# Kernel tuning notes

Measured on AMD Instinct MI355X. Metric: run time of the kernel, lower is better.

## Reference

```python
import jax, jax.numpy as jnp
import numpy as np

B, H, W = 2, 32, 128
HW = H * W
N, C = 4096, 64
KQ, KN = 32, 16          # nsample_q, nsample
DIST = 10.0              # neighbor distance threshold
NEG = -1e10


def _knn(q, p, k):
    # q: (B,M,3), p: (B,N,3) -> idx (B,M,k), sqdist (B,M,k)
    sqd = jnp.sum((q[:, :, None, :] - p[:, None, :, :]) ** 2, axis=-1)
    neg, idx = jax.lax.top_k(-sqd, k)
    return idx, -neg


def _gather(p, idx):
    # p: (B,N,C), idx: (B,M,K) -> (B,M,K,C)
    return jax.vmap(lambda a, i: a[i])(p, idx)


def _norm_feat(x):
    # per-point channel normalization, torch.std default is unbiased (ddof=1)
    m = jnp.mean(x, axis=-1, keepdims=True)
    s = jnp.clip(jnp.std(x, axis=-1, keepdims=True, ddof=1), 1e-12)
    return (x - m) / s


def _conv(x, w, b, g, e):
    # 1x1 conv + BatchNorm (track_running_stats=False -> batch stats) + LeakyReLU(0.1)
    y = jnp.einsum('bnkc,cd->bnkd', x, w) + b
    mu = y.mean(axis=(0, 1, 2), keepdims=True)
    var = y.var(axis=(0, 1, 2), keepdims=True)
    y = (y - mu) * jax.lax.rsqrt(var + 1e-5) * g + e
    return jnp.where(y > 0, y, 0.1 * y)


def setup_inputs() -> dict:
    key = jax.random.key(0)
    ks = jax.random.split(key, 20)
    inp = {
        'xyz_proj_raw': jax.random.normal(ks[0], (B, H, W, 3), jnp.float32),
        'warped_xyz': jax.random.normal(ks[1], (B, HW, 3), jnp.float32),
        'warped_points': jax.random.normal(ks[2], (B, HW, C), jnp.float32),
        'idx_n2': jax.random.randint(ks[3], (B, HW, 2), 0, W),
        'f2_xyz': jax.random.normal(ks[4], (B, N, 3), jnp.float32),
        'f2_points': jax.random.normal(ks[5], (B, N, C), jnp.float32),
        'lidar_z': jax.random.uniform(ks[6], (B, HW, 1), jnp.float32),
    }
    shapes = {
        'm1w0': (70, 128), 'm1w1': (128, 64), 'piw': (6, 64),
        'm2w0': (128, 64), 'm2w1': (64, 64), 'pcw': (10, 64),
        'm3w0': (192, 64), 'm3w1': (64, 64),
    }
    i = 7
    for name, shp in shapes.items():
        inp[name] = jax.random.normal(ks[i], shp, jnp.float32) * 0.05
        i += 1
        pre = name[:-2] if name[-2] == 'w' else name[:-1]
        suf = name[-1] if name[-2] == 'w' else ''
        cout = shp[1]
        inp[pre + 'b' + suf] = jnp.zeros((cout,), jnp.float32)
        inp[pre + 'g' + suf] = jnp.ones((cout,), jnp.float32)
        inp[pre + 'e' + suf] = jnp.zeros((cout,), jnp.float32)
    return inp


def reference(xyz_proj_raw, warped_xyz, warped_points, idx_n2, f2_xyz, f2_points, lidar_z,
              m1w0, m1b0, m1g0, m1e0, m1w1, m1b1, m1g1, m1e1,
              piw, pib, pig, pie,
              m2w0, m2b0, m2g0, m2e0, m2w1, m2b1, m2g1, m2e1,
              pcw, pcb, pcg, pce,
              m3w0, m3b0, m3g0, m3e0, m3w1, m3b1, m3g1, m3e1):
    # ---- stage 1: cross kNN grouping into image features ----
    idx_q, _ = _knn(warped_xyz, f2_xyz, KQ)
    qi_xyz = _gather(f2_xyz, idx_q)          # (B,HW,KQ,3)
    qi_pts = _gather(f2_points, idx_q)       # (B,HW,KQ,C)

    wxyz = warped_xyz * lidar_z              # (B,HW,3)
    pi_xyz_exp = jnp.broadcast_to(wxyz[:, :, None, :], (B, HW, KQ, 3))
    pi_pts_exp = jnp.broadcast_to(warped_points[:, :, None, :], (B, HW, KQ, C))
    pi_xyz_diff_concat = jnp.concatenate([pi_xyz_exp, qi_xyz], axis=3)  # (B,HW,KQ,6)

    pi_feat_diff = _norm_feat(pi_pts_exp) * _norm_feat(qi_pts)          # correlation
    feat = jnp.concatenate([pi_xyz_diff_concat, pi_feat_diff], axis=3)  # (B,HW,KQ,70)

    feat = _conv(feat, m1w0, m1b0, m1g0, m1e0)
    feat = _conv(feat, m1w1, m1b1, m1g1, m1e1)                          # (B,HW,KQ,64)
    pi_enc = _conv(pi_xyz_diff_concat, piw, pib, pig, pie)              # (B,HW,KQ,64)

    pi_cat = jnp.concatenate([pi_enc, feat], axis=3)
    pi_cat = _conv(pi_cat, m2w0, m2b0, m2g0, m2e0)
    pi_cat = _conv(pi_cat, m2w1, m2b1, m2g1, m2e1)
    WQ = jax.nn.softmax(pi_cat, axis=2)
    pi_feat1 = jnp.sum(WQ * feat, axis=2)                               # (B,HW,64)

    # ---- stage 2: self kNN (use_trans=False -> raw projected xyz), thresholded validity ----
    xyz_pr = xyz_proj_raw.reshape(B, HW, 3)
    idx2, sqd2 = _knn(xyz_pr, xyz_pr, KN)
    valid = (sqd2 < DIST * DIST).astype(pi_feat1.dtype)[..., None]      # (B,HW,KN,1)

    pc_xyz_g = _gather(wxyz, idx2)                                      # (B,HW,KN,3)
    pc_pts_g = _gather(pi_feat1, idx2)                                  # (B,HW,KN,64)
    pc_xyz_new = jnp.broadcast_to(wxyz[:, :, None, :], (B, HW, KN, 3))
    pc_pts_new = jnp.broadcast_to(warped_points[:, :, None, :], (B, HW, KN, C))

    pc_diff = pc_xyz_g - pc_xyz_new
    pc_euc = jnp.sqrt(jnp.sum(pc_diff * pc_diff, axis=3, keepdims=True) + 1e-20)
    pc_xyz_cat = jnp.concatenate([pc_xyz_new, pc_xyz_g, pc_diff, pc_euc], axis=3)  # 10ch

    pc_enc = _conv(pc_xyz_cat, pcw, pcb, pcg, pce)
    pc_cat = jnp.concatenate([pc_enc, pc_pts_new, pc_pts_g], axis=-1)   # (B,HW,KN,192)
    pc_cat = _conv(pc_cat, m3w0, m3b0, m3g0, m3e0)
    pc_cat = _conv(pc_cat, m3w1, m3b1, m3g1, m3e1)

    pc_cat = pc_cat * valid + NEG * (1.0 - valid)
    WP = jax.nn.softmax(pc_cat, axis=2)
    out = jnp.sum(WP * pc_pts_g, axis=2)                                # (B,HW,64)
    return out.reshape(B, H, W, -1)
```

## Files before the change

kernel.cpp:

```cpp
#include <hip/hip_runtime.h>
#include <math.h>

constexpr int Bn  = 2;
constexpr int HWn = 4096;
constexpr int Nn  = 4096;
constexpr int KQn = 32;
constexpr int KNn = 16;
constexpr float INV_R1 = 1.0f/262144.0f;
constexpr float INV_R2 = 1.0f/131072.0f;

typedef _Float16 f16x8 __attribute__((ext_vector_type(8)));
typedef _Float16 f16x2 __attribute__((ext_vector_type(2)));
typedef float    f32x4 __attribute__((ext_vector_type(4)));

__device__ __forceinline__ float wred64(float v){
  #pragma unroll
  for (int m = 32; m > 0; m >>= 1) v += __shfl_xor(v, m, 64);
  return v;
}
__device__ __forceinline__ float leakyf(float v){ return v > 0.f ? v : 0.1f*v; }

__device__ __forceinline__ void bn_param(const float* st, int c, float inv_n,
                                         const float* g, const float* e,
                                         float& sc, float& sh){
  float mu  = st[c]*inv_n;
  float var = st[128+c]*inv_n - mu*mu;
  float s   = g[c]*rsqrtf(var + 1e-5f);
  sc = s; sh = e[c] - mu*s;
}

__device__ __forceinline__ void build_x70(int row,
    const float* __restrict__ wxyz, const float* __restrict__ f2_xyz,
    const float* __restrict__ normW, const float* __restrict__ normF2,
    const int* __restrict__ idxq, float* x){
  int p = row >> 5;
  int b = p >> 12;
  int idx = idxq[row];
  const float* wx = wxyz + (size_t)p*3;
  const float* fx = f2_xyz + ((size_t)b*Nn + idx)*3;
  x[0]=wx[0]; x[1]=wx[1]; x[2]=wx[2];
  x[3]=fx[0]; x[4]=fx[1]; x[5]=fx[2];
  const float4* nw = (const float4*)(normW  + (size_t)p*64);
  const float4* nf = (const float4*)(normF2 + ((size_t)b*Nn + idx)*64);
  #pragma unroll
  for (int c=0;c<16;c++){
    float4 a = nw[c], q = nf[c];
    x[6+4*c+0]=a.x*q.x; x[6+4*c+1]=a.y*q.y; x[6+4*c+2]=a.z*q.z; x[6+4*c+3]=a.w*q.w;
  }
}

__device__ __forceinline__ void build_x10(int row,
    const float* __restrict__ wxyz, const int* __restrict__ idx2, float* x){
  int p = row >> 4, b = p >> 12;
  int idx = idx2[row];
  const float* nw = wxyz + (size_t)p*3;
  const float* gw = wxyz + ((size_t)b*HWn + idx)*3;
  float n0=nw[0],n1=nw[1],n2=nw[2];
  float g0=gw[0],g1=gw[1],g2=gw[2];
  float d0=g0-n0, d1=g1-n1, d2=g2-n2;
  x[0]=n0;x[1]=n1;x[2]=n2; x[3]=g0;x[4]=g1;x[5]=g2;
  x[6]=d0;x[7]=d1;x[8]=d2; x[9]=sqrtf(d0*d0+d1*d1+d2*d2+1e-20f);
}

__global__ __launch_bounds__(256) void k_knn_prep(
    const float* __restrict__ qA, const float* __restrict__ pA, int* __restrict__ oA,
    const float* __restrict__ qB, const float* __restrict__ pB, int* __restrict__ oB,
    float* __restrict__ ovalid,
    const float* __restrict__ lidar_z,
    const float* __restrict__ warped_points, const float* __restrict__ f2_points,
    const float* __restrict__ m1w0, const float* __restrict__ m1w1,
    const float* __restrict__ piw, const float* __restrict__ pcw,
    const float* __restrict__ m2w0, const float* __restrict__ m2w1,
    const float* __restrict__ m3w0, const float* __restrict__ m3w1,
    float* __restrict__ wxyz, float* __restrict__ normW, float* __restrict__ normF2,
    float* __restrict__ piwT, float* __restrict__ pcwT,
    _Float16* __restrict__ w1h, _Float16* __restrict__ w2h,
    _Float16* __restrict__ w3h, _Float16* __restrict__ w4h,
    _Float16* __restrict__ w5h, _Float16* __restrict__ w6h)
{
  int bid = blockIdx.x;
  int tid = threadIdx.x;
  if (bid >= 16384){
    int blk = bid - 16384;
    if (blk < 4096){
      int lane = tid & 63;
      int p = blk*4 + (tid >> 6);
      const float* src; float* dst;
      if (p < Bn*HWn){ src = warped_points + (size_t)p*64; dst = normW + (size_t)p*64; }
      else { int q = p - Bn*HWn; src = f2_points + (size_t)q*64; dst = normF2 + (size_t)q*64; }
      float x = src[lane];
      float m = wred64(x) * (1.f/64.f);
      float d = x - m;
      float ss = wred64(d*d);
      float s = fmaxf(sqrtf(ss*(1.f/63.f)), 1e-12f);
      dst[lane] = d / s;
    } else if (blk < 4192){
      int e = (blk-4096)*256 + tid;
      wxyz[e] = qA[e] * lidar_z[e/3];
    } else if (blk < 4196){
      int e = (blk-4192)*256 + tid;
      if (e < 384){ piwT[(e & 63)*6  + (e >> 6)] = piw[e]; }
      else if (e < 1024){ int f = e-384; pcwT[(f & 63)*10 + (f >> 6)] = pcw[f]; }
    } else {
      int e = (blk-4196)*256 + tid;
      if (e < 12288){
        int j = e/96, k = e - j*96;
        w1h[e] = (k < 70) ? (_Float16)m1w0[k*128 + j] : (_Float16)0.f;
      } else if (e < 20480){
        int f = e - 12288; int d = f >> 7, c = f & 127;
        w2h[f] = (_Float16)m1w1[c*64 + d];
      } else if (e < 28672){
        int f = e - 20480; int d = f >> 7, c = f & 127;
        w3h[f] = (_Float16)m2w0[c*64 + d];
      } else if (e < 32768){
        int f = e - 28672; int d = f >> 6, c = f & 63;
        w4h[f] = (_Float16)m2w1[c*64 + d];
      } else if (e < 45056){
        int f = e - 32768; int d = f/192, c = f - 192*d;
        w5h[f] = (_Float16)m3w0[c*64 + d];
      } else {
        int f = e - 45056; int d = f >> 6, c = f & 63;
        w6h[f] = (_Float16)m3w1[c*64 + d];
      }
    }
    return;
  }
  __shared__ int hist[4096];
  __shared__ int wsum[4];
  __shared__ unsigned int redm[4], redM[4];
  __shared__ int sh_sel, sh_rem, sh_cls, cnt_lt, cnt_eq;
  bool second = bid >= 8192;
  int blk = second ? (bid - 8192) : bid;
  int K = second ? KNn : KQn;
  const float* qpts = second ? qB : qA;
  const float* pts  = second ? pB : pA;
  int* oidx = second ? oB : oA;
  int b = blk >> 12;
  int qi = blk & 4095;
  int lane = tid & 63, wv = tid >> 6;
  const float* qp = qpts + ((size_t)(b*HWn+qi))*3;
  float qx=qp[0], qy=qp[1], qz=qp[2];
  const float* pb = pts + (size_t)b*Nn*3;
  unsigned int key[16];
  {
    const float4* pb4 = (const float4*)(pb + (size_t)tid*48);
    float4 v[12];
    #pragma unroll
    for (int i=0;i<12;i++) v[i] = pb4[i];
    const float* f = (const float*)v;
    #pragma unroll
    for (int i=0;i<16;i++){
      float dx = __fsub_rn(qx, f[i*3+0]);
      float dy = __fsub_rn(qy, f[i*3+1]);
      float dz = __fsub_rn(qz, f[i*3+2]);
      float d2 = __fadd_rn(__fadd_rn(__fmul_rn(dx,dx), __fmul_rn(dy,dy)), __fmul_rn(dz,dz));
      key[i] = __float_as_uint(d2);
    }
  }
  {
    int4 z = {0,0,0,0};
    #pragma unroll
    for (int j=0;j<4;j++) ((int4*)hist)[tid + j*256] = z;
  }
  unsigned int mn = key[0], mx = key[0];
  #pragma unroll
  for (int i=1;i<16;i++){ mn = min(mn, key[i]); mx = max(mx, key[i]); }
  #pragma unroll
  for (int m=32;m>0;m>>=1){
    mn = min(mn, (unsigned int)__shfl_xor((int)mn, m, 64));
    mx = max(mx, (unsigned int)__shfl_xor((int)mx, m, 64));
  }
  if (lane == 0){ redm[wv] = mn; redM[wv] = mx; }
  if (tid == 0){ cnt_lt = 0; cnt_eq = 0; }
  __syncthreads();
  mn = min(min(redm[0],redm[1]), min(redm[2],redm[3]));
  mx = max(max(redM[0],redM[1]), max(redM[2],redM[3]));
  unsigned int R = mx - mn;
  int L = (R == 0u) ? 0 : (31 - __clz(R));
  int shift = (L > 11) ? (L - 11) : 0;
  #pragma unroll
  for (int i=0;i<16;i++){
    unsigned int d = ((key[i]-mn) >> shift) & 4095u;
    int slot = (int)(((d & 15u) << 8) | (d >> 4));
    atomicAdd(&hist[slot], 1);
  }
  __syncthreads();
  {
    int hv[16]; int tot = 0;
    #pragma unroll
    for (int i=0;i<16;i++){ hv[i] = hist[tid + i*256]; tot += hv[i]; }
    int pref = tot;
    #pragma unroll
    for (int m=1;m<64;m<<=1){ int t = __shfl_up(pref, m, 64); if (lane >= m) pref += t; }
    if (lane == 63) wsum[wv] = pref;
    __syncthreads();
    int off = 0;
    #pragma unroll
    for (int i=0;i<3;i++) if (i < wv) off += wsum[i];
    pref += off;
    if (pref >= K && (pref - tot) < K){
      int running = pref - tot;
      bool done = false;
      #pragma unroll
      for (int i=0;i<16;i++){
        if (!done && running + hv[i] >= K){
          sh_sel = tid*16 + i;
          sh_rem = K - running;
          sh_cls = hv[i];
          done = true;
        }
        if (!done) running += hv[i];
      }
    }
  }
  __syncthreads();
  unsigned int sel = (unsigned int)sh_sel;
  int rem = sh_rem, cls = sh_cls;
  int nless = K - rem;
  size_t obase = ((size_t)(b*HWn+qi))*K;
  const unsigned int U100 = __float_as_uint(100.0f);
  #pragma unroll
  for (int i=0;i<16;i++){
    unsigned int d = ((key[i]-mn) >> shift) & 4095u;
    if (d < sel){
      int s = atomicAdd(&cnt_lt, 1);
      oidx[obase+s] = tid*16 + i;
      if (second) ovalid[obase+s] = (key[i] < U100) ? 1.f : 0.f;
    } else if (d == sel){
      int s = atomicAdd(&cnt_eq, 1);
      if (s < 2048){ hist[s] = (int)key[i]; hist[2048+s] = tid*16 + i; }
    }
  }
  __syncthreads();
  if (wv == 0){
    int cc = cls < 2048 ? cls : 2048;
    for (int c = lane; c < cc; c += 64){
      unsigned int kc = (unsigned int)hist[c];
      int ic = hist[2048+c];
      int rank = 0;
      for (int j = 0; j < cc; j++){
        unsigned int kj = (unsigned int)hist[j];
        if (kj < kc || (kj == kc && hist[2048+j] < ic)) rank++;
      }
      if (rank < rem){
        oidx[obase + nless + rank] = ic;
        if (second) ovalid[obase + nless + rank] = (kc < U100) ? 1.f : 0.f;
      }
    }
  }
}

__global__ __launch_bounds__(256) void k_build_stats(
    const float* __restrict__ wxyz, const float* __restrict__ f2_xyz,
    const float* __restrict__ normW, const float* __restrict__ normF2,
    const int* __restrict__ idxq, const int* __restrict__ idx2,
    const _Float16* __restrict__ w1h,
    _Float16* __restrict__ X1, float* stats, float* __restrict__ gram)
{
  __shared__ float ssum[128], sssq[128];
  __shared__ float sacc[66];
  int blk = blockIdx.x, tid = threadIdx.x, lane = tid & 63;
  if (blk < 1024){
    int row = blk*256 + tid;
    {
      float x[70];
      build_x70(row, wxyz, f2_xyz, normW, normF2, idxq, x);
      unsigned int* d32 = (unsigned int*)(X1 + (size_t)row*96);
      union { unsigned int u; _Float16 h[2]; } pk;
      #pragma unroll
      for (int c=0;c<35;c++){
        pk.h[0] = (_Float16)x[2*c]; pk.h[1] = (_Float16)x[2*c+1];
        d32[c] = pk.u;
      }
      #pragma unroll
      for (int c=35;c<48;c++) d32[c] = 0u;
    }
    if (tid < 128){ ssum[tid]=0.f; sssq[tid]=0.f; }
    __syncthreads();
    int wave = tid >> 6;
    int quad = lane >> 4, n16 = lane & 15;
    float r1[8], r2[8];
    #pragma unroll
    for (int i=0;i<8;i++){ r1[i]=0.f; r2[i]=0.f; }
    for (int t=0;t<4;t++){
      int m0 = blk*256 + t*64 + wave*16;
      const _Float16* xr = X1 + (size_t)(m0 + n16)*96 + quad*8;
      f16x8 a0 = *(const f16x8*)(xr);
      f16x8 a1 = *(const f16x8*)(xr + 32);
      f16x8 a2 = *(const f16x8*)(xr + 64);
      #pragma unroll
      for (int nt = 0; nt < 8; nt++){
        const _Float16* wr = w1h + (size_t)(nt*16 + n16)*96 + quad*8;
        f16x8 b0 = *(const f16x8*)(wr);
        f16x8 b1 = *(const f16x8*)(wr + 32);
        f16x8 b2 = *(const f16x8*)(wr + 64);
        f32x4 acc = {0.f,0.f,0.f,0.f};
        acc = __builtin_amdgcn_mfma_f32_16x16x32_f16(a0, b0, acc, 0,0,0);
        acc = __builtin_amdgcn_mfma_f32_16x16x32_f16(a1, b1, acc, 0,0,0);
        acc = __builtin_amdgcn_mfma_f32_16x16x32_f16(a2, b2, acc, 0,0,0);
        float s1 = acc[0]+acc[1]+acc[2]+acc[3];
        float s2 = acc[0]*acc[0]+acc[1]*acc[1]+acc[2]*acc[2]+acc[3]*acc[3];
        s1 += __shfl_xor(s1, 16, 64); s1 += __shfl_xor(s1, 32, 64);
        s2 += __shfl_xor(s2, 16, 64); s2 += __shfl_xor(s2, 32, 64);
        r1[nt] += s1; r2[nt] += s2;
      }
    }
    if (quad == 0){
      #pragma unroll
      for (int nt=0;nt<8;nt++){
        atomicAdd(&ssum[nt*16+n16], r1[nt]); atomicAdd(&sssq[nt*16+n16], r2[nt]);
      }
    }
    __syncthreads();
    if (tid < 128){ atomicAdd(&stats[tid], ssum[tid]); atomicAdd(&stats[128+tid], sssq[tid]); }
  } else if (blk < 1088){
    float a[28];
    #pragma unroll
    for (int q=0;q<28;q++) a[q]=0.f;
    int g = (blk-1024)*256 + tid;
    for (int s=0;s<16;s++){
      int row = g + s*16384;
      int p = row >> 5, b = p >> 12;
      int idx = idxq[row];
      const float* wx = wxyz + (size_t)p*3;
      const float* fx = f2_xyz + ((size_t)b*Nn + idx)*3;
      float xt[7] = {wx[0],wx[1],wx[2],fx[0],fx[1],fx[2],1.f};
      int q=0;
      #pragma unroll
      for (int i=0;i<7;i++)
        #pragma unroll
        for (int j=i;j<7;j++) a[q++] += xt[i]*xt[j];
    }
    if (tid < 28) sacc[tid]=0.f;
    __syncthreads();
    #pragma unroll
    for (int q=0;q<28;q++){
      float v = wred64(a[q]);
      if (lane==0) atomicAdd(&sacc[q], v);
    }
    __syncthreads();
    if (tid < 28) atomicAdd(&gram[tid], sacc[tid]);
  } else {
    float a[66];
    #pragma unroll
    for (int q=0;q<66;q++) a[q]=0.f;
    int g = (blk-1088)*256 + tid;
    for (int s=0;s<16;s++){
      int row = g + s*8192;
      float x[10];
      build_x10(row, wxyz, idx2, x);
      float xt[11] = {x[0],x[1],x[2],x[3],x[4],x[5],x[6],x[7],x[8],x[9],1.f};
      int q=0;
      #pragma unroll
      for (int i=0;i<11;i++)
        #pragma unroll
        for (int j=i;j<11;j++) a[q++] += xt[i]*xt[j];
    }
    if (tid < 66) sacc[tid]=0.f;
    __syncthreads();
    #pragma unroll
    for (int q=0;q<66;q++){
      float v = wred64(a[q]);
      if (lane==0) atomicAdd(&sacc[q], v);
    }
    __syncthreads();
    if (tid < 66) atomicAdd(&gram[32+tid], sacc[tid]);
  }
}

__global__ __launch_bounds__(256) void k_mfma_m1(
    const _Float16* __restrict__ X1, const _Float16* __restrict__ w1h,
    const _Float16* __restrict__ w2h,
    const float* __restrict__ m1g0, const float* __restrict__ m1e0,
    float* stats, _Float16* __restrict__ y2h,
    const float* __restrict__ gram,
    const float* __restrict__ piw, const float* __restrict__ pib,
    const float* __restrict__ pcw, const float* __restrict__ pcb)
{
  if (blockIdx.x >= 1024){
    int tid = threadIdx.x;
    if (tid < 64){
      int c = tid;
      float wt[7];
      #pragma unroll
      for (int i=0;i<6;i++) wt[i] = piw[i*64+c];
      wt[6] = pib[c];
      const float* G = gram;
      float sum=0.f, ssq=0.f;
      #pragma unroll
      for (int i=0;i<7;i++){
        int offi = i*7 - (i*(i-1))/2;
        sum += wt[i]*G[offi + (6-i)];
        #pragma unroll
        for (int j=0;j<7;j++){
          int ii = i<j? i : j, jj = i<j? j : i;
          int o = ii*7 - (ii*(ii-1))/2 + (jj-ii);
          ssq += wt[i]*wt[j]*G[o];
        }
      }
      stats[2*256+c] = sum; stats[2*256+128+c] = ssq;
    } else if (tid < 128){
      int c = tid-64;
      float wt[11];
      #pragma unroll
      for (int i=0;i<10;i++) wt[i] = pcw[i*64+c];
      wt[10] = pcb[c];
      const float* G = gram + 32;
      float sum=0.f, ssq=0.f;
      #pragma unroll
      for (int i=0;i<11;i++){
        int offi = i*11 - (i*(i-1))/2;
        sum += wt[i]*G[offi + (10-i)];
        #pragma unroll
        for (int j=0;j<11;j++){
          int ii = i<j? i : j, jj = i<j? j : i;
          int o = ii*11 - (ii*(ii-1))/2 + (jj-ii);
          ssq += wt[i]*wt[j]*G[o];
        }
      }
      stats[5*256+c] = sum; stats[5*256+128+c] = ssq;
    }
    return;
  }
  __shared__ _Float16 st[64*136];
  __shared__ float sc1[128], sh1[128], ssum[64], sssq[64];
  int tid = threadIdx.x;
  if (tid < 128){
    float s,h; bn_param(stats, tid, INV_R1, m1g0, m1e0, s, h);
    sc1[tid]=s; sh1[tid]=h;
  }
  if (tid < 64){ ssum[tid]=0.f; sssq[tid]=0.f; }
  __syncthreads();
  int wave = tid >> 6, lane = tid & 63;
  int quad = lane >> 4, n16 = lane & 15;
  float r1[4], r2[4];
  #pragma unroll
  for (int i=0;i<4;i++){ r1[i]=0.f; r2[i]=0.f; }
  for (int t=0;t<4;t++){
    int m0 = blockIdx.x*256 + t*64 + wave*16;
    const _Float16* xr = X1 + (size_t)(m0 + n16)*96 + quad*8;
    f16x8 a0 = *(const f16x8*)(xr);
    f16x8 a1 = *(const f16x8*)(xr + 32);
    f16x8 a2 = *(const f16x8*)(xr + 64);
    #pragma unroll
    for (int nt = 0; nt < 8; nt++){
      const _Float16* wr = w1h + (size_t)(nt*16 + n16)*96 + quad*8;
      f16x8 b0 = *(const f16x8*)(wr);
      f16x8 b1 = *(const f16x8*)(wr + 32);
      f16x8 b2 = *(const f16x8*)(wr + 64);
      f32x4 acc = {0.f,0.f,0.f,0.f};
      acc = __builtin_amdgcn_mfma_f32_16x16x32_f16(a0, b0, acc, 0,0,0);
      acc = __builtin_amdgcn_mfma_f32_16x16x32_f16(a1, b1, acc, 0,0,0);
      acc = __builtin_amdgcn_mfma_f32_16x16x32_f16(a2, b2, acc, 0,0,0);
      int ch = nt*16 + n16;
      float sc = sc1[ch], sh = sh1[ch];
      #pragma unroll
      for (int r=0;r<4;r++){
        float v = leakyf(acc[r]*sc + sh);
        st[(size_t)(wave*16 + quad*4 + r)*136 + ch] = (_Float16)v;
      }
    }
    __syncthreads();
    const _Float16* tr = st + (size_t)(wave*16 + n16)*136 + quad*8;
    f16x8 t0 = *(const f16x8*)(tr);
    f16x8 t1 = *(const f16x8*)(tr + 32);
    f16x8 t2 = *(const f16x8*)(tr + 64);
    f16x8 t3 = *(const f16x8*)(tr + 96);
    #pragma unroll
    for (int nt = 0; nt < 4; nt++){
      const _Float16* wr = w2h + (size_t)(nt*16 + n16)*128 + quad*8;
      f16x8 b0 = *(const f16x8*)(wr);
      f16x8 b1 = *(const f16x8*)(wr + 32);
      f16x8 b2 = *(const f16x8*)(wr + 64);
      f16x8 b3 = *(const f16x8*)(wr + 96);
      f32x4 acc = {0.f,0.f,0.f,0.f};
      acc = __builtin_amdgcn_mfma_f32_16x16x32_f16(t0, b0, acc, 0,0,0);
      acc = __builtin_amdgcn_mfma_f32_16x16x32_f16(t1, b1, acc, 0,0,0);
      acc = __builtin_amdgcn_mfma_f32_16x16x32_f16(t2, b2, acc, 0,0,0);
      acc = __builtin_amdgcn_mfma_f32_16x16x32_f16(t3, b3, acc, 0,0,0);
      int ch = nt*16 + n16;
      #pragma unroll
      for (int r=0;r<4;r++){
        int rowg = blockIdx.x*256 + t*64 + wave*16 + quad*4 + r;
        y2h[(size_t)rowg*64 + ch] = (_Float16)acc[r];
      }
      float s1 = acc[0]+acc[1]+acc[2]+acc[3];
      float s2 = acc[0]*acc[0]+acc[1]*acc[1]+acc[2]*acc[2]+acc[3]*acc[3];
      s1 += __shfl_xor(s1, 16, 64); s1 += __shfl_xor(s1, 32, 64);
      s2 += __shfl_xor(s2, 16, 64); s2 += __shfl_xor(s2, 32, 64);
      r1[nt] += s1; r2[nt] += s2;
    }
    __syncthreads();
  }
  if (quad == 0){
    #pragma unroll
    for (int nt=0;nt<4;nt++){
      atomicAdd(&ssum[nt*16+n16], r1[nt]); atomicAdd(&sssq[nt*16+n16], r2[nt]);
    }
  }
  __syncthreads();
  if (tid < 64){ atomicAdd(&stats[1*256+tid], ssum[tid]); atomicAdd(&stats[1*256+128+tid], sssq[tid]); }
}

__global__ __launch_bounds__(256) void k_mfma_m2a(
    const float* __restrict__ wxyz, const float* __restrict__ f2_xyz,
    const int* __restrict__ idxq,
    const float* __restrict__ piwT, const float* __restrict__ pib,
    const float* __restrict__ pig, const float* __restrict__ pie,
    const float* __restrict__ m1g1, const float* __restrict__ m1e1,
    const _Float16* __restrict__ y2h, const _Float16* __restrict__ w3h,
    float* stats, _Float16* __restrict__ y3h)
{
  __shared__ _Float16 su[64*136];
  __shared__ float spw[384];
  __shared__ float scp[64], shp[64], sc2[64], sh2[64], ssum[64], sssq[64];
  int tid = threadIdx.x;
  for (int d = tid; d < 384; d += 256) spw[d] = piwT[d];
  if (tid < 64){
    float s,h;
    bn_param(stats+2*256, tid, INV_R1, pig,  pie,  s, h); scp[tid]=s; shp[tid]=h;
    bn_param(stats+1*256, tid, INV_R1, m1g1, m1e1, s, h); sc2[tid]=s; sh2[tid]=h;
    ssum[tid]=0.f; sssq[tid]=0.f;
  }
  __syncthreads();
  int r = tid & 63, cg = tid >> 6;
  int wave = tid >> 6, lane = tid & 63, quad = lane >> 4, n16 = lane & 15;
  float r1[4], r2[4];
  #pragma unroll
  for (int i=0;i<4;i++){ r1[i]=0.f; r2[i]=0.f; }
  for (int t=0;t<4;t++){
    int rowg = blockIdx.x*256 + t*64 + r;
    {
      int p = rowg >> 5, b = p >> 12;
      int idx = idxq[rowg];
      const float* wx = wxyz + (size_t)p*3;
      const float* fx = f2_xyz + ((size_t)b*Nn + idx)*3;
      float x0=wx[0],x1=wx[1],x2=wx[2],x3=fx[0],x4=fx[1],x5=fx[2];
      #pragma unroll
      for (int jj=0;jj<16;jj++){
        int j = cg*16 + jj;
        const float* pw = spw + j*6;
        float e = pib[j] + x0*pw[0]+x1*pw[1]+x2*pw[2]+x3*pw[3]+x4*pw[4]+x5*pw[5];
        su[r*136 + j] = (_Float16)leakyf(e*scp[j] + shp[j]);
      }
      const f16x8* yr = (const f16x8*)(y2h + (size_t)rowg*64 + cg*16);
      f16x8 q0 = yr[0], q1 = yr[1];
      #pragma unroll
      for (int jj=0;jj<8;jj++){
        int c = cg*16 + jj;
        su[r*136 + 64 + c] = (_Float16)leakyf((float)q0[jj]*sc2[c] + sh2[c]);
      }
      #pragma unroll
      for (int jj=0;jj<8;jj++){
        int c = cg*16 + 8 + jj;
        su[r*136 + 64 + c] = (_Float16)leakyf((float)q1[jj]*sc2[c] + sh2[c]);
      }
    }
    __syncthreads();
    const _Float16* ur = su + (size_t)(wave*16 + n16)*136 + quad*8;
    f16x8 a0 = *(const f16x8*)(ur);
    f16x8 a1 = *(const f16x8*)(ur + 32);
    f16x8 a2 = *(const f16x8*)(ur + 64);
    f16x8 a3 = *(const f16x8*)(ur + 96);
    #pragma unroll
    for (int nt = 0; nt < 4; nt++){
      const _Float16* wr = w3h + (size_t)(nt*16 + n16)*128 + quad*8;
      f16x8 b0 = *(const f16x8*)(wr);
      f16x8 b1 = *(const f16x8*)(wr + 32);
      f16x8 b2 = *(const f16x8*)(wr + 64);
      f16x8 b3 = *(const f16x8*)(wr + 96);
      f32x4 acc = {0.f,0.f,0.f,0.f};
      acc = __builtin_amdgcn_mfma_f32_16x16x32_f16(a0, b0, acc, 0,0,0);
      acc = __builtin_amdgcn_mfma_f32_16x16x32_f16(a1, b1, acc, 0,0,0);
      acc = __builtin_amdgcn_mfma_f32_16x16x32_f16(a2, b2, acc, 0,0,0);
      acc = __builtin_amdgcn_mfma_f32_16x16x32_f16(a3, b3, acc, 0,0,0);
      int ch = nt*16 + n16;
      #pragma unroll
      for (int rr=0;rr<4;rr++){
        int rg = blockIdx.x*256 + t*64 + wave*16 + quad*4 + rr;
        y3h[(size_t)rg*64 + ch] = (_Float16)acc[rr];
      }
      float s1 = acc[0]+acc[1]+acc[2]+acc[3];
      float s2 = acc[0]*acc[0]+acc[1]*acc[1]+acc[2]*acc[2]+acc[3]*acc[3];
      s1 += __shfl_xor(s1, 16, 64); s1 += __shfl_xor(s1, 32, 64);
      s2 += __shfl_xor(s2, 16, 64); s2 += __shfl_xor(s2, 32, 64);
      r1[nt] += s1; r2[nt] += s2;
    }
    __syncthreads();
  }
  if (quad == 0){
    #pragma unroll
    for (int nt=0;nt<4;nt++){
      atomicAdd(&ssum[nt*16+n16], r1[nt]); atomicAdd(&sssq[nt*16+n16], r2[nt]);
    }
  }
  __syncthreads();
  if (tid < 64){ atomicAdd(&stats[3*256+tid], ssum[tid]); atomicAdd(&stats[3*256+128+tid], sssq[tid]); }
}

__global__ __launch_bounds__(256) void k_mfma_pw64(
    const _Float16* __restrict__ yin, const _Float16* __restrict__ wh,
    const float* __restrict__ g, const float* __restrict__ e,
    const float* statsIn, float* statsOut, float inv_n,
    _Float16* __restrict__ yout)
{
  __shared__ _Float16 stt[64*72];
  __shared__ float sc[64], sh[64], ssum[64], sssq[64];
  int tid = threadIdx.x;
  if (tid < 64){
    float s,h; bn_param(statsIn, tid, inv_n, g, e, s, h);
    sc[tid]=s; sh[tid]=h; ssum[tid]=0.f; sssq[tid]=0.f;
  }
  __syncthreads();
  int r = tid & 63, cg = tid >> 6;
  int wave = tid >> 6, lane = tid & 63, quad = lane >> 4, n16 = lane & 15;
  float r1[4], r2[4];
  #pragma unroll
  for (int i=0;i<4;i++){ r1[i]=0.f; r2[i]=0.f; }
  for (int t=0;t<4;t++){
    int rowg = blockIdx.x*256 + t*64 + r;
    const f16x8* yr = (const f16x8*)(yin + (size_t)rowg*64 + cg*16);
    f16x8 q0 = yr[0], q1 = yr[1];
    #pragma unroll
    for (int jj=0;jj<8;jj++){
      int c = cg*16 + jj;
      stt[r*72 + c] = (_Float16)leakyf((float)q0[jj]*sc[c] + sh[c]);
    }
    #pragma unroll
    for (int jj=0;jj<8;jj++){
      int c = cg*16 + 8 + jj;
      stt[r*72 + c] = (_Float16)leakyf((float)q1[jj]*sc[c] + sh[c]);
    }
    __syncthreads();
    const _Float16* tr = stt + (size_t)(wave*16 + n16)*72 + quad*8;
    f16x8 a0 = *(const f16x8*)(tr);
    f16x8 a1 = *(const f16x8*)(tr + 32);
    #pragma unroll
    for (int nt = 0; nt < 4; nt++){
      const _Float16* wr = wh + (size_t)(nt*16 + n16)*64 + quad*8;
      f16x8 b0 = *(const f16x8*)(wr);
      f16x8 b1 = *(const f16x8*)(wr + 32);
      f32x4 acc = {0.f,0.f,0.f,0.f};
      acc = __builtin_amdgcn_mfma_f32_16x16x32_f16(a0, b0, acc, 0,0,0);
      acc = __builtin_amdgcn_mfma_f32_16x16x32_f16(a1, b1, acc, 0,0,0);
      int ch = nt*16 + n16;
      #pragma unroll
      for (int rr=0;rr<4;rr++){
        int rg = blockIdx.x*256 + t*64 + wave*16 + quad*4 + rr;
        yout[(size_t)rg*64 + ch] = (_Float16)acc[rr];
      }
      float s1 = acc[0]+acc[1]+acc[2]+acc[3];
      float s2 = acc[0]*acc[0]+acc[1]*acc[1]+acc[2]*acc[2]+acc[3]*acc[3];
      s1 += __shfl_xor(s1, 16, 64); s1 += __shfl_xor(s1, 32, 64);
      s2 += __shfl_xor(s2, 16, 64); s2 += __shfl_xor(s2, 32, 64);
      r1[nt] += s1; r2[nt] += s2;
    }
    __syncthreads();
  }
  if (quad == 0){
    #pragma unroll
    for (int nt=0;nt<4;nt++){
      atomicAdd(&ssum[nt*16+n16], r1[nt]); atomicAdd(&sssq[nt*16+n16], r2[nt]);
    }
  }
  __syncthreads();
  if (tid < 64){ atomicAdd(&statsOut[tid], ssum[tid]); atomicAdd(&statsOut[128+tid], sssq[tid]); }
}

__global__ __launch_bounds__(256) void k_mfma_m3a(
    const float* __restrict__ wxyz, const float* __restrict__ warped_points,
    const _Float16* __restrict__ pif1h, const int* __restrict__ idx2,
    const float* __restrict__ pcwT, const float* __restrict__ pcb,
    const float* __restrict__ pcg, const float* __restrict__ pce,
    const _Float16* __restrict__ w5h,
    float* stats, _Float16* __restrict__ y5h)
{
  __shared__ _Float16 sv[64*200];
  __shared__ float spw[640];
  __shared__ float scp[64], shp[64], ssum[64], sssq[64];
  int tid = threadIdx.x;
  for (int d = tid; d < 640; d += 256) spw[d] = pcwT[d];
  if (tid < 64){
    float s,h; bn_param(stats+5*256, tid, INV_R2, pcg, pce, s, h);
    scp[tid]=s; shp[tid]=h; ssum[tid]=0.f; sssq[tid]=0.f;
  }
  __syncthreads();
  int r = tid & 63, cg = tid >> 6;
  int wave = tid >> 6, lane = tid & 63, quad = lane >> 4, n16 = lane & 15;
  float r1[4], r2[4];
  #pragma unroll
  for (int i=0;i<4;i++){ r1[i]=0.f; r2[i]=0.f; }
  for (int t=0;t<4;t++){
    int rowg = blockIdx.x*256 + t*64 + r;
    {
      int p = rowg >> 4, b = p >> 12;
      int idx = idx2[rowg];
      float x[10];
      build_x10(rowg, wxyz, idx2, x);
      #pragma unroll
      for (int jj=0;jj<16;jj++){
        int j = cg*16 + jj;
        const float* pw = spw + j*10;
        float e = pcb[j];
        #pragma unroll
        for (int i=0;i<10;i++) e += x[i]*pw[i];
        sv[r*200 + j] = (_Float16)leakyf(e*scp[j] + shp[j]);
      }
      const float4* wp = (const float4*)(warped_points + (size_t)p*64 + cg*16);
      #pragma unroll
      for (int v4=0; v4<4; v4++){
        float4 q = wp[v4];
        int c = 64 + cg*16 + v4*4;
        sv[r*200 + c + 0] = (_Float16)q.x;
        sv[r*200 + c + 1] = (_Float16)q.y;
        sv[r*200 + c + 2] = (_Float16)q.z;
        sv[r*200 + c + 3] = (_Float16)q.w;
      }
      const f16x8* pg = (const f16x8*)(pif1h + ((size_t)(b*HWn) + idx)*64 + cg*16);
      f16x8 g0 = pg[0], g1 = pg[1];
      #pragma unroll
      for (int jj=0;jj<8;jj++) sv[r*200 + 128 + cg*16 + jj] = g0[jj];
      #pragma unroll
      for (int jj=0;jj<8;jj++) sv[r*200 + 136 + cg*16 + jj] = g1[jj];
    }
    __syncthreads();
    const _Float16* vr = sv + (size_t)(wave*16 + n16)*200 + quad*8;
    f16x8 a0 = *(const f16x8*)(vr);
    f16x8 a1 = *(const f16x8*)(vr + 32);
    f16x8 a2 = *(const f16x8*)(vr + 64);
    f16x8 a3 = *(const f16x8*)(vr + 96);
    f16x8 a4 = *(const f16x8*)(vr + 128);
    f16x8 a5 = *(const f16x8*)(vr + 160);
    #pragma unroll
    for (int nt = 0; nt < 4; nt++){
      const _Float16* wr = w5h + (size_t)(nt*16 + n16)*192 + quad*8;
      f32x4 acc = {0.f,0.f,0.f,0.f};
      acc = __builtin_amdgcn_mfma_f32_16x16x32_f16(a0, *(const f16x8*)(wr),       acc, 0,0,0);
      acc = __builtin_amdgcn_mfma_f32_16x16x32_f16(a1, *(const f16x8*)(wr + 32),  acc, 0,0,0);
      acc = __builtin_amdgcn_mfma_f32_16x16x32_f16(a2, *(const f16x8*)(wr + 64),  acc, 0,0,0);
      acc = __builtin_amdgcn_mfma_f32_16x16x32_f16(a3, *(const f16x8*)(wr + 96),  acc, 0,0,0);
      acc = __builtin_amdgcn_mfma_f32_16x16x32_f16(a4, *(const f16x8*)(wr + 128), acc, 0,0,0);
      acc = __builtin_amdgcn_mfma_f32_16x16x32_f16(a5, *(const f16x8*)(wr + 160), acc, 0,0,0);
      int ch = nt*16 + n16;
      #pragma unroll
      for (int rr=0;rr<4;rr++){
        int rg = blockIdx.x*256 + t*64 + wave*16 + quad*4 + rr;
        y5h[(size_t)rg*64 + ch] = (_Float16)acc[rr];
      }
      float s1 = acc[0]+acc[1]+acc[2]+acc[3];
      float s2 = acc[0]*acc[0]+acc[1]*acc[1]+acc[2]*acc[2]+acc[3]*acc[3];
      s1 += __shfl_xor(s1, 16, 64); s1 += __shfl_xor(s1, 32, 64);
      s2 += __shfl_xor(s2, 16, 64); s2 += __shfl_xor(s2, 32, 64);
      r1[nt] += s1; r2[nt] += s2;
    }
    __syncthreads();
  }
  if (quad == 0){
    #pragma unroll
    for (int nt=0;nt<4;nt++){
      atomicAdd(&ssum[nt*16+n16], r1[nt]); atomicAdd(&sssq[nt*16+n16], r2[nt]);
    }
  }
  __syncthreads();
  if (tid < 64){ atomicAdd(&stats[6*256+tid], ssum[tid]); atomicAdd(&stats[6*256+128+tid], sssq[tid]); }
}

__global__ __launch_bounds__(256) void k_softmax1(
    const _Float16* __restrict__ y2h, const _Float16* __restrict__ y4h,
    const float* stats,
    const float* __restrict__ m1g1, const float* __restrict__ m1e1,
    const float* __restrict__ m2g1, const float* __restrict__ m2e1,
    _Float16* __restrict__ pif1h)
{
  int tid = threadIdx.x;
  int p  = blockIdx.x*8 + (tid >> 5);
  int dp = tid & 31;
  int d0 = 2*dp, d1 = 2*dp + 1;
  float sc2a,sh2a,sc4a,sh4a, sc2b,sh2b,sc4b,sh4b;
  bn_param(stats+1*256, d0, INV_R1, m1g1, m1e1, sc2a, sh2a);
  bn_param(stats+4*256, d0, INV_R1, m2g1, m2e1, sc4a, sh4a);
  bn_param(stats+1*256, d1, INV_R1, m1g1, m1e1, sc2b, sh2b);
  bn_param(stats+4*256, d1, INV_R1, m2g1, m2e1, sc4b, sh4b);
  size_t rb = (size_t)p*KQn;
  const _Float16* y4base = y4h + rb*64 + d0;
  const _Float16* y2base = y2h + rb*64 + d0;
  float va[32], vb[32];
  float mxa = -1e30f, mxb = -1e30f;
  #pragma unroll
  for (int k=0;k<32;k++){
    f16x2 h = *(const f16x2*)(y4base + (size_t)k*64);
    float ta = leakyf((float)h[0]*sc4a + sh4a);
    float tb = leakyf((float)h[1]*sc4b + sh4b);
    va[k] = ta; mxa = fmaxf(mxa, ta);
    vb[k] = tb; mxb = fmaxf(mxb, tb);
  }
  float sea = 0.f, seb = 0.f;
  #pragma unroll
  for (int k=0;k<32;k++){
    float ea = __expf(va[k]-mxa); va[k]=ea; sea += ea;
    float eb = __expf(vb[k]-mxb); vb[k]=eb; seb += eb;
  }
  float inva = 1.f/sea, invb = 1.f/seb;
  float acca = 0.f, accb = 0.f;
  #pragma unroll
  for (int k=0;k<32;k++){
    f16x2 h = *(const f16x2*)(y2base + (size_t)k*64);
    acca += va[k]*leakyf((float)h[0]*sc2a + sh2a);
    accb += vb[k]*leakyf((float)h[1]*sc2b + sh2b);
  }
  f16x2 o; o[0] = (_Float16)(acca*inva); o[1] = (_Float16)(accb*invb);
  *(f16x2*)(pif1h + (size_t)p*64 + d0) = o;
}

__global__ __launch_bounds__(256) void k_softmax2(
    const _Float16* __restrict__ y6h, const _Float16* __restrict__ pif1h,
    const int* __restrict__ idx2, const float* __restrict__ validf,
    const float* stats,
    const float* __restrict__ m3g1, const float* __restrict__ m3e1,
    float* __restrict__ out)
{
  int tid = threadIdx.x;
  int p  = blockIdx.x*8 + (tid >> 5);
  int b  = p >> 12;
  int dp = tid & 31;
  int d0 = 2*dp, d1 = 2*dp + 1;
  float sca,sha,scb,shb;
  bn_param(stats+7*256, d0, INV_R2, m3g1, m3e1, sca, sha);
  bn_param(stats+7*256, d1, INV_R2, m3g1, m3e1, scb, shb);
  size_t rb = (size_t)p*KNn;
  const _Float16* y6base = y6h + rb*64 + d0;
  float va[16], vb[16];
  float mxa = -1e30f, mxb = -1e30f;
  #pragma unroll
  for (int k=0;k<16;k++){
    f16x2 h = *(const f16x2*)(y6base + (size_t)k*64);
    bool ok = validf[rb+k] > 0.5f;
    float ta = ok ? leakyf((float)h[0]*sca + sha) : -1e10f;
    float tb = ok ? leakyf((float)h[1]*scb + shb) : -1e10f;
    va[k] = ta; mxa = fmaxf(mxa, ta);
    vb[k] = tb; mxb = fmaxf(mxb, tb);
  }
  float sea = 0.f, seb = 0.f;
  #pragma unroll
  for (int k=0;k<16;k++){
    float ea = __expf(va[k]-mxa); va[k]=ea; sea += ea;
    float eb = __expf(vb[k]-mxb); vb[k]=eb; seb += eb;
  }
  float inva = 1.f/sea, invb = 1.f/seb;
  float acca = 0.f, accb = 0.f;
  #pragma unroll
  for (int k=0;k<16;k++){
    int idx = idx2[rb+k];
    f16x2 h = *(const f16x2*)(pif1h + ((size_t)(b*HWn) + idx)*64 + d0);
    acca += va[k]*(float)h[0];
    accb += vb[k]*(float)h[1];
  }
  float2 o; o.x = acca*inva; o.y = accb*invb;
  *(float2*)(out + (size_t)p*64 + d0) = o;
}

extern "C" void kernel_launch(void* const* d_in, const int* in_sizes, int n_in,
                              void* d_out, int out_size, void* d_ws, size_t ws_size,
                              hipStream_t stream)
{
  (void)in_sizes; (void)n_in; (void)out_size; (void)ws_size;
  const float* xyz_proj      = (const float*)d_in[0];
  const float* warped_xyz    = (const float*)d_in[1];
  const float* warped_points = (const float*)d_in[2];
  const float* f2_xyz        = (const float*)d_in[4];
  const float* f2_points     = (const float*)d_in[5];
  const float* lidar_z       = (const float*)d_in[6];
  const float* m1w0=(const float*)d_in[7],  *m1g0=(const float*)d_in[9],  *m1e0=(const float*)d_in[10];
  const float* m1w1=(const float*)d_in[11], *m1g1=(const float*)d_in[13], *m1e1=(const float*)d_in[14];
  const float* piw =(const float*)d_in[15], *pib =(const float*)d_in[16], *pig =(const float*)d_in[17], *pie =(const float*)d_in[18];
  const float* m2w0=(const float*)d_in[19], *m2g0=(const float*)d_in[21], *m2e0=(const float*)d_in[22];
  const float* m2w1=(const float*)d_in[23], *m2g1=(const float*)d_in[25], *m2e1=(const float*)d_in[26];
  const float* pcw =(const float*)d_in[27], *pcb =(const float*)d_in[28], *pcg =(const float*)d_in[29], *pce =(const float*)d_in[30];
  const float* m3w0=(const float*)d_in[31], *m3g0=(const float*)d_in[33], *m3e0=(const float*)d_in[34];
  const float* m3w1=(const float*)d_in[35], *m3g1=(const float*)d_in[37], *m3e1=(const float*)d_in[38];
  float* out = (float*)d_out;

  float* ws     = (float*)d_ws;
  float* wxyz   = ws;
  float* normW  = wxyz   + 24576;
  float* normF2 = normW  + 524288;
  float* piwT   = normF2 + 524288;
  float* pcwT   = piwT   + 384;
  float* stats  = pcwT   + 640;
  float* gram   = stats  + 2048;
  int*   idxq   = (int*)(gram + 128);
  int*   idx2   = idxq   + 262144;
  float* validf = (float*)(idx2 + 131072);
  _Float16* pif1h = (_Float16*)(validf + 131072);
  float* X1f    = validf + 131072 + 524288;
  _Float16* X1  = (_Float16*)X1f;
  float* y2f    = X1f + 12582912;
  _Float16* y2h = (_Float16*)y2f;
  float* y3f    = y2f + 8388608;
  _Float16* y3h = (_Float16*)y3f;
  float* whb    = y3f + 8388608;
  _Float16* w1h = (_Float16*)whb;
  _Float16* w2h = w1h + 12288;
  _Float16* w3h = w2h + 8192;
  _Float16* w4h = w3h + 8192;
  _Float16* w5h = w4h + 4096;
  _Float16* w6h = w5h + 12288;
  _Float16* y4h = (_Float16*)X1f;
  _Float16* y5h = (_Float16*)(X1f + 8388608);
  _Float16* y6h = y3h;

  hipMemsetAsync(stats, 0, (2048+128)*sizeof(float), stream);
  k_knn_prep<<<20772,256,0,stream>>>(warped_xyz, f2_xyz, idxq,
                                     xyz_proj, xyz_proj, idx2, validf,
                                     lidar_z, warped_points, f2_points,
                                     m1w0, m1w1, piw, pcw, m2w0, m2w1, m3w0, m3w1,
                                     wxyz, normW, normF2, piwT, pcwT,
                                     w1h, w2h, w3h, w4h, w5h, w6h);
  k_build_stats<<<1120,256,0,stream>>>(wxyz, f2_xyz, normW, normF2, idxq, idx2,
                                       w1h, X1, stats, gram);
  k_mfma_m1<<<1025,256,0,stream>>>(X1, w1h, w2h, m1g0, m1e0, stats, y2h,
                                   gram, piw, pib, pcw, pcb);
  k_mfma_m2a<<<1024,256,0,stream>>>(wxyz, f2_xyz, idxq, piwT, pib, pig, pie,
                                    m1g1, m1e1, y2h, w3h, stats, y3h);
  k_mfma_pw64<<<1024,256,0,stream>>>(y3h, w4h, m2g0, m2e0,
                                     stats+3*256, stats+4*256, INV_R1, y4h);
  k_softmax1<<<1024,256,0,stream>>>(y2h, y4h, stats, m1g1, m1e1, m2g1, m2e1, pif1h);
  k_mfma_m3a<<<512,256,0,stream>>>(wxyz, warped_points, pif1h, idx2,
                                   pcwT, pcb, pcg, pce, w5h, stats, y5h);
  k_mfma_pw64<<<512,256,0,stream>>>(y5h, w6h, m3g0, m3e0,
                                    stats+6*256, stats+7*256, INV_R2, y6h);
  k_softmax2<<<1024,256,0,stream>>>(y6h, pif1h, idx2, validf, stats, m3g1, m3e1, out);
}
```

Baseline: 495.0 us.

## Build 70-channel input tiles in shared memory instead of materializing X1 globally

Removes the global X1 fp16 buffer (262144 rows x 96 halves) that k_build_stats wrote and k_mfma_m1 read back. Both kernels now rebuild each 64-row input tile cooperatively in LDS, with four threads per row gathering normW/normF2 products and xyz. This trades a large global write and read for recomputing the gathers twice and extra LDS usage and barriers per tile. It also changes the barrier placement in k_mfma_m1.

```diff
diff --git a/kernel.cpp b/kernel.cpp
--- a/kernel.cpp
+++ b/kernel.cpp
@@ -29,23 +29,37 @@
   sc = s; sh = e[c] - mu*s;
 }
 
-__device__ __forceinline__ void build_x70(int row,
-    const float* __restrict__ wxyz, const float* __restrict__ f2_xyz,
+constexpr int XT_LD = 104;
+__device__ __forceinline__ void build_xtile(
+    int m0, const float* __restrict__ wxyz, const float* __restrict__ f2_xyz,
     const float* __restrict__ normW, const float* __restrict__ normF2,
-    const int* __restrict__ idxq, float* x){
-  int p = row >> 5;
-  int b = p >> 12;
+    const int* __restrict__ idxq, _Float16* __restrict__ xt, int tid)
+{
+  int r = tid >> 2, q = tid & 3;
+  int row = m0 + r;
+  int p = row >> 5, b = p >> 12;
   int idx = idxq[row];
-  const float* wx = wxyz + (size_t)p*3;
-  const float* fx = f2_xyz + ((size_t)b*Nn + idx)*3;
-  x[0]=wx[0]; x[1]=wx[1]; x[2]=wx[2];
-  x[3]=fx[0]; x[4]=fx[1]; x[5]=fx[2];
-  const float4* nw = (const float4*)(normW  + (size_t)p*64);
-  const float4* nf = (const float4*)(normF2 + ((size_t)b*Nn + idx)*64);
-  #pragma unroll
-  for (int c=0;c<16;c++){
-    float4 a = nw[c], q = nf[c];
-    x[6+4*c+0]=a.x*q.x; x[6+4*c+1]=a.y*q.y; x[6+4*c+2]=a.z*q.z; x[6+4*c+3]=a.w*q.w;
+  unsigned int* d32 = (unsigned int*)(xt + r*XT_LD);
+  union { unsigned int u; _Float16 h[2]; } pk;
+  if (q == 0){
+    const float* wx = wxyz + (size_t)p*3;
+    const float* fx = f2_xyz + ((size_t)b*Nn + idx)*3;
+    pk.h[0]=(_Float16)wx[0]; pk.h[1]=(_Float16)wx[1]; d32[0]=pk.u;
+    pk.h[0]=(_Float16)wx[2]; pk.h[1]=(_Float16)fx[0]; d32[1]=pk.u;
+    pk.h[0]=(_Float16)fx[1]; pk.h[1]=(_Float16)fx[2]; d32[2]=pk.u;
+  }
+  const float4* nw = (const float4*)(normW  + (size_t)p*64) + q*4;
+  const float4* nf = (const float4*)(normF2 + ((size_t)b*Nn + idx)*64) + q*4;
+  #pragma unroll
+  for (int i=0;i<4;i++){
+    float4 a = nw[i], f = nf[i];
+    int base = 3 + q*8 + i*2;
+    pk.h[0]=(_Float16)(a.x*f.x); pk.h[1]=(_Float16)(a.y*f.y); d32[base]=pk.u;
+    pk.h[0]=(_Float16)(a.z*f.z); pk.h[1]=(_Float16)(a.w*f.w); d32[base+1]=pk.u;
+  }
+  if (q == 3){
+    #pragma unroll
+    for (int c=35;c<48;c++) d32[c] = 0u;
   }
 }
 
@@ -255,36 +269,23 @@
     const float* __restrict__ normW, const float* __restrict__ normF2,
     const int* __restrict__ idxq, const int* __restrict__ idx2,
     const _Float16* __restrict__ w1h,
-    _Float16* __restrict__ X1, float* stats, float* __restrict__ gram)
+    float* stats, float* __restrict__ gram)
 {
-  __shared__ float ssum[128], sssq[128];
   __shared__ float sacc[66];
   int blk = blockIdx.x, tid = threadIdx.x, lane = tid & 63;
   if (blk < 1024){
-    int row = blk*256 + tid;
-    {
-      float x[70];
-      build_x70(row, wxyz, f2_xyz, normW, normF2, idxq, x);
-      unsigned int* d32 = (unsigned int*)(X1 + (size_t)row*96);
-      union { unsigned int u; _Float16 h[2]; } pk;
-      #pragma unroll
-      for (int c=0;c<35;c++){
-        pk.h[0] = (_Float16)x[2*c]; pk.h[1] = (_Float16)x[2*c+1];
-        d32[c] = pk.u;
-      }
-      #pragma unroll
-      for (int c=35;c<48;c++) d32[c] = 0u;
-    }
+    __shared__ _Float16 xt[64*XT_LD];
+    __shared__ float ssum[128], sssq[128];
     if (tid < 128){ ssum[tid]=0.f; sssq[tid]=0.f; }
-    __syncthreads();
     int wave = tid >> 6;
     int quad = lane >> 4, n16 = lane & 15;
     float r1[8], r2[8];
     #pragma unroll
     for (int i=0;i<8;i++){ r1[i]=0.f; r2[i]=0.f; }
     for (int t=0;t<4;t++){
-      int m0 = blk*256 + t*64 + wave*16;
-      const _Float16* xr = X1 + (size_t)(m0 + n16)*96 + quad*8;
+      build_xtile(blk*256 + t*64, wxyz, f2_xyz, normW, normF2, idxq, xt, tid);
+      __syncthreads();
+      const _Float16* xr = xt + (size_t)(wave*16 + n16)*XT_LD + quad*8;
       f16x8 a0 = *(const f16x8*)(xr);
       f16x8 a1 = *(const f16x8*)(xr + 32);
       f16x8 a2 = *(const f16x8*)(xr + 64);
@@ -304,6 +305,7 @@
         s2 += __shfl_xor(s2, 16, 64); s2 += __shfl_xor(s2, 32, 64);
         r1[nt] += s1; r2[nt] += s2;
       }
+      __syncthreads();
     }
     if (quad == 0){
       #pragma unroll
@@ -324,12 +326,12 @@
       int idx = idxq[row];
       const float* wx = wxyz + (size_t)p*3;
       const float* fx = f2_xyz + ((size_t)b*Nn + idx)*3;
-      float xt[7] = {wx[0],wx[1],wx[2],fx[0],fx[1],fx[2],1.f};
+      float xt7[7] = {wx[0],wx[1],wx[2],fx[0],fx[1],fx[2],1.f};
       int q=0;
       #pragma unroll
       for (int i=0;i<7;i++)
         #pragma unroll
-        for (int j=i;j<7;j++) a[q++] += xt[i]*xt[j];
+        for (int j=i;j<7;j++) a[q++] += xt7[i]*xt7[j];
     }
     if (tid < 28) sacc[tid]=0.f;
     __syncthreads();
@@ -349,12 +351,12 @@
       int row = g + s*8192;
       float x[10];
       build_x10(row, wxyz, idx2, x);
-      float xt[11] = {x[0],x[1],x[2],x[3],x[4],x[5],x[6],x[7],x[8],x[9],1.f};
+      float xt11[11] = {x[0],x[1],x[2],x[3],x[4],x[5],x[6],x[7],x[8],x[9],1.f};
       int q=0;
       #pragma unroll
       for (int i=0;i<11;i++)
         #pragma unroll
-        for (int j=i;j<11;j++) a[q++] += xt[i]*xt[j];
+        for (int j=i;j<11;j++) a[q++] += xt11[i]*xt11[j];
     }
     if (tid < 66) sacc[tid]=0.f;
     __syncthreads();
@@ -369,8 +371,10 @@
 }
 
 __global__ __launch_bounds__(256) void k_mfma_m1(
-    const _Float16* __restrict__ X1, const _Float16* __restrict__ w1h,
-    const _Float16* __restrict__ w2h,
+    const float* __restrict__ wxyz, const float* __restrict__ f2_xyz,
+    const float* __restrict__ normW, const float* __restrict__ normF2,
+    const int* __restrict__ idxq,
+    const _Float16* __restrict__ w1h, const _Float16* __restrict__ w2h,
     const float* __restrict__ m1g0, const float* __restrict__ m1e0,
     float* stats, _Float16* __restrict__ y2h,
     const float* __restrict__ gram,
@@ -422,6 +426,7 @@
     }
     return;
   }
+  __shared__ _Float16 xt[64*XT_LD];
   __shared__ _Float16 st[64*136];
   __shared__ float sc1[128], sh1[128], ssum[64], sssq[64];
   int tid = threadIdx.x;
@@ -430,15 +435,15 @@
     sc1[tid]=s; sh1[tid]=h;
   }
   if (tid < 64){ ssum[tid]=0.f; sssq[tid]=0.f; }
-  __syncthreads();
   int wave = tid >> 6, lane = tid & 63;
   int quad = lane >> 4, n16 = lane & 15;
   float r1[4], r2[4];
   #pragma unroll
   for (int i=0;i<4;i++){ r1[i]=0.f; r2[i]=0.f; }
   for (int t=0;t<4;t++){
-    int m0 = blockIdx.x*256 + t*64 + wave*16;
-    const _Float16* xr = X1 + (size_t)(m0 + n16)*96 + quad*8;
+    build_xtile(blockIdx.x*256 + t*64, wxyz, f2_xyz, normW, normF2, idxq, xt, tid);
+    __syncthreads();
+    const _Float16* xr = xt + (size_t)(wave*16 + n16)*XT_LD + quad*8;
     f16x8 a0 = *(const f16x8*)(xr);
     f16x8 a1 = *(const f16x8*)(xr + 32);
     f16x8 a2 = *(const f16x8*)(xr + 64);
@@ -490,8 +495,8 @@
       s2 += __shfl_xor(s2, 16, 64); s2 += __shfl_xor(s2, 32, 64);
       r1[nt] += s1; r2[nt] += s2;
     }
-    __syncthreads();
-  }
+  }
+  __syncthreads();
   if (quad == 0){
     #pragma unroll
     for (int nt=0;nt<4;nt++){
@@ -893,7 +898,6 @@
   float* validf = (float*)(idx2 + 131072);
   _Float16* pif1h = (_Float16*)(validf + 131072);
   float* X1f    = validf + 131072 + 524288;
-  _Float16* X1  = (_Float16*)X1f;
   float* y2f    = X1f + 12582912;
   _Float16* y2h = (_Float16*)y2f;
   float* y3f    = y2f + 8388608;
@@ -917,8 +921,9 @@
                                      wxyz, normW, normF2, piwT, pcwT,
                                      w1h, w2h, w3h, w4h, w5h, w6h);
   k_build_stats<<<1120,256,0,stream>>>(wxyz, f2_xyz, normW, normF2, idxq, idx2,
-                                       w1h, X1, stats, gram);
-  k_mfma_m1<<<1025,256,0,stream>>>(X1, w1h, w2h, m1g0, m1e0, stats, y2h,
+                                       w1h, stats, gram);
+  k_mfma_m1<<<1025,256,0,stream>>>(wxyz, f2_xyz, normW, normF2, idxq,
+                                   w1h, w2h, m1g0, m1e0, stats, y2h,
                                    gram, piw, pib, pcw, pcb);
   k_mfma_m2a<<<1024,256,0,stream>>>(wxyz, f2_xyz, idxq, piwT, pib, pig, pie,
                                     m1g1, m1e1, y2h, w3h, stats, y3h);
```

New measurement: 490.7 us. No clear change (-0.9%).
